# Optimization experiments

Hardware: AMD Instinct MI355X
Metric: run time of the kernel (lower is better)

## Reference

```python
import jax, jax.numpy as jnp
import numpy as np


def _layernorm(x, g, b, eps=1e-5):
    mu = x.mean(-1, keepdims=True)
    var = ((x - mu) ** 2).mean(-1, keepdims=True)
    return (x - mu) / jnp.sqrt(var + eps) * g + b


def _bilinear_sample(feat, coords):
    # feat: (B,C,H,W,D); coords: (B,C,N,2) normalized to [-1,1]
    # torch.grid_sample(mode='bilinear', padding_mode='zeros', align_corners=True)
    B, C, H, W, D = feat.shape
    x = (coords[..., 0] + 1.0) * 0.5 * (W - 1)  # grid x -> width axis
    y = (coords[..., 1] + 1.0) * 0.5 * (H - 1)  # grid y -> height axis
    x0 = jnp.floor(x)
    y0 = jnp.floor(y)
    wx1 = x - x0
    wy1 = y - y0
    bi = jnp.arange(B)[:, None, None]
    ci = jnp.arange(C)[None, :, None]

    def corner(yi, xi, w):
        inb = (xi >= 0) & (xi < W) & (yi >= 0) & (yi < H)
        xc = jnp.clip(xi, 0, W - 1).astype(jnp.int32)
        yc = jnp.clip(yi, 0, H - 1).astype(jnp.int32)
        v = feat[bi, ci, yc, xc]  # (B,C,N,D) gather
        return v * (w * inb)[..., None]

    return (corner(y0, x0, (1 - wy1) * (1 - wx1))
            + corner(y0, x0 + 1, (1 - wy1) * wx1)
            + corner(y0 + 1, x0, wy1 * (1 - wx1))
            + corner(y0 + 1, x0 + 1, wy1 * wx1))


def setup_inputs() -> dict:
    key = jax.random.key(0)
    ks = jax.random.split(key, 12)
    B, C, N, D, H, W = 2, 8, 16384, 256, 64, 64
    s = 1.0 / np.sqrt(D).astype(np.float32)
    return {
        "queries": jax.random.normal(ks[0], (B, N, D), jnp.float32),
        "image_features": jax.random.normal(ks[1], (B, C, H, W, D), jnp.float32),
        "pixel_coords": jax.random.uniform(ks[2], (B, C, N, 2), jnp.float32) * 2.0 - 1.0,
        "valid_mask": jax.random.randint(ks[3], (B, C, N), 0, 2).astype(jnp.int32),
        "Wq": jax.random.normal(ks[4], (D, D), jnp.float32) * s,
        "bq": jnp.zeros((D,), jnp.float32),
        "Wkv": jax.random.normal(ks[5], (D, 2 * D), jnp.float32) * s,
        "bkv": jnp.zeros((2 * D,), jnp.float32),
        "Wo": jax.random.normal(ks[6], (D, D), jnp.float32) * s,
        "bo": jnp.zeros((D,), jnp.float32),
        "gamma": jnp.ones((D,), jnp.float32),
        "beta": jnp.zeros((D,), jnp.float32),
    }


def reference(queries, image_features, pixel_coords, valid_mask,
              Wq, bq, Wkv, bkv, Wo, bo, gamma, beta):
    B, N, D = queries.shape
    residual = queries
    qn = _layernorm(queries, gamma, beta)
    sampled = _bilinear_sample(image_features, pixel_coords)      # (B,C,N,D)
    sampled = jnp.transpose(sampled, (0, 2, 1, 3))                 # (B,N,C,D)
    q = qn @ Wq + bq                                               # (B,N,D)
    kv = sampled @ Wkv + bkv                                       # (B,N,C,2D)
    k, v = kv[..., :D], kv[..., D:]
    scores = jnp.einsum('bnd,bncd->bnc', q, k) / jnp.sqrt(jnp.float32(D))
    valid = jnp.transpose(valid_mask, (0, 2, 1)) != 0              # (B,N,C)
    scores = jnp.where(valid, scores, -jnp.inf)
    attn = jax.nn.softmax(scores, axis=-1)
    attn = jnp.where(jnp.isnan(attn), 0.0, attn)                   # all-invalid -> 0
    out = jnp.einsum('bnc,bncd->bnd', attn, v)
    return residual + out @ Wo + bo
```

## Files before the change

### kernel.cpp

```cpp
#include <hip/hip_runtime.h>
#include <math.h>

#define NROWS 32768

typedef __attribute__((ext_vector_type(8))) short short8;
typedef __attribute__((ext_vector_type(4))) float f32x4;

#define WS_ABF    0
#define WS_WVOBF  32768
#define WS_PB     65536
#define WS_BVO    65792
#define WS_FEATBF 8487424

__device__ __forceinline__ unsigned short f2bf(float f) {
    unsigned u = __builtin_bit_cast(unsigned, f);
    u += 0x7FFFu + ((u >> 16) & 1u);
    return (unsigned short)(u >> 16);
}
__device__ __forceinline__ float bf_lo(unsigned u) {
    return __builtin_bit_cast(float, u << 16);
}
__device__ __forceinline__ float bf_hi(unsigned u) {
    return __builtin_bit_cast(float, u & 0xFFFF0000u);
}

__global__ __launch_bounds__(256)
void precompute_kernel(const float* __restrict__ Wq, const float* __restrict__ bq,
                       const float* __restrict__ Wkv, const float* __restrict__ bkv,
                       const float* __restrict__ Wo, const float* __restrict__ feat,
                       float* __restrict__ ws) {
    int t = threadIdx.x;
    int blk = blockIdx.x;
    if (blk >= 514) {
        long i = (long)(blk - 514) * 4096 + t * 16;
        const float4* src = (const float4*)(feat + i);
        unsigned short* dst = (unsigned short*)(ws + WS_FEATBF) + i;
        #pragma unroll
        for (int h = 0; h < 2; ++h) {
            float4 a = src[2 * h], b = src[2 * h + 1];
            uint4 o;
            o.x = (unsigned)f2bf(a.x) | ((unsigned)f2bf(a.y) << 16);
            o.y = (unsigned)f2bf(a.z) | ((unsigned)f2bf(a.w) << 16);
            o.z = (unsigned)f2bf(b.x) | ((unsigned)f2bf(b.y) << 16);
            o.w = (unsigned)f2bf(b.z) | ((unsigned)f2bf(b.w) << 16);
            *(uint4*)(dst + 8 * h) = o;
        }
        return;
    }
    if (blk < 256) {
        int f = blk;
        const float4* wq4 = (const float4*)(Wq + f * 256);
        const float4* wk4 = (const float4*)(Wkv + (long)t * 512);
        float acc = 0.f;
        #pragma unroll 8
        for (int d4 = 0; d4 < 64; ++d4) {
            float4 a = wq4[d4], b = wk4[d4];
            acc += a.x * b.x + a.y * b.y + a.z * b.z + a.w * b.w;
        }
        ((unsigned short*)(ws + WS_ABF))[t * 256 + f] = f2bf(acc);
    } else if (blk < 512) {
        int e = blk - 256;
        float acc = 0.f;
        #pragma unroll 8
        for (int g = 0; g < 256; ++g)
            acc = fmaf(Wkv[(long)e * 512 + 256 + g], Wo[g * 256 + t], acc);
        ((unsigned short*)(ws + WS_WVOBF))[t * 256 + e] = f2bf(acc);
    } else if (blk == 512) {
        float acc = 0.f;
        #pragma unroll 8
        for (int d = 0; d < 256; ++d)
            acc = fmaf(bq[d], Wkv[(long)t * 512 + d], acc);
        ws[WS_PB + t] = acc;
    } else {
        float acc = 0.f;
        #pragma unroll 8
        for (int g = 0; g < 256; ++g)
            acc = fmaf(bkv[256 + g], Wo[g * 256 + t], acc);
        ws[WS_BVO + t] = acc;
    }
}

#define RPB  32
#define SLOT 260

__global__ __launch_bounds__(512, 8)
void fused_rowpipe(const float* __restrict__ queries, const float* __restrict__ gamma,
                   const float* __restrict__ beta, const float* __restrict__ coords,
                   const int* __restrict__ vmask, const float* __restrict__ bo,
                   const float* __restrict__ ws, float* __restrict__ out) {
    __shared__ float buf[RPB * SLOT + RPB];
    float* ssu = buf + RPB * SLOT;

    const unsigned short* Abf    = (const unsigned short*)(ws + WS_ABF);
    const unsigned short* Wvobf  = (const unsigned short*)(ws + WS_WVOBF);
    const float*          pb     = ws + WS_PB;
    const float*          bvo    = ws + WS_BVO;
    const unsigned short* featbf = (const unsigned short*)(ws + WS_FEATBF);

    int tid = threadIdx.x, wave = tid >> 6, lane = tid & 63;
    long row0 = (long)blockIdx.x * RPB;

    float4 qstash[4];

    {
        float4 g4 = *(const float4*)(gamma + 4 * lane);
        float4 b4 = *(const float4*)(beta + 4 * lane);
        #pragma unroll
        for (int rr = 0; rr < 4; ++rr) {
            int r = wave * 4 + rr;
            float4 v = *(const float4*)(queries + (row0 + r) * 256 + 4 * lane);
            qstash[rr] = v;
            float s = v.x + v.y + v.z + v.w;
            s += __shfl_xor(s, 32); s += __shfl_xor(s, 16); s += __shfl_xor(s, 8);
            s += __shfl_xor(s, 4);  s += __shfl_xor(s, 2);  s += __shfl_xor(s, 1);
            float mu = s * 0.00390625f;
            float dx = v.x - mu, dy = v.y - mu, dz = v.z - mu, dw = v.w - mu;
            float vv = dx * dx + dy * dy + dz * dz + dw * dw;
            vv += __shfl_xor(vv, 32); vv += __shfl_xor(vv, 16); vv += __shfl_xor(vv, 8);
            vv += __shfl_xor(vv, 4);  vv += __shfl_xor(vv, 2);  vv += __shfl_xor(vv, 1);
            float rstd = rsqrtf(vv * 0.00390625f + 1e-5f);
            float qx = dx * rstd * g4.x + b4.x;
            float qy = dy * rstd * g4.y + b4.y;
            float qz = dz * rstd * g4.z + b4.z;
            float qw = dw * rstd * g4.w + b4.w;
            unsigned lo = (unsigned)f2bf(qx) | ((unsigned)f2bf(qy) << 16);
            unsigned hi = (unsigned)f2bf(qz) | ((unsigned)f2bf(qw) << 16);
            *(uint2*)((unsigned short*)&buf[r * SLOT] + 4 * lane) = make_uint2(lo, hi);
        }
    }
    __syncthreads();

    int r16 = lane & 15, g = lane >> 4;
    f32x4 zero = {0.f, 0.f, 0.f, 0.f};

    {
        f32x4 acc[2][2];
        #pragma unroll
        for (int mt = 0; mt < 2; ++mt)
            #pragma unroll
            for (int nt = 0; nt < 2; ++nt) acc[mt][nt] = zero;

        #pragma unroll
        for (int ks = 0; ks < 8; ++ks) {
            short8 bfr[2], afr[2];
            #pragma unroll
            for (int nt = 0; nt < 2; ++nt)
                bfr[nt] = *(const short8*)(Abf + ((wave * 32 + nt * 16 + r16) << 8) + ks * 32 + g * 8);
            #pragma unroll
            for (int mt = 0; mt < 2; ++mt)
                afr[mt] = *(const short8*)((const unsigned short*)buf + (mt * 16 + r16) * (SLOT * 2) + ks * 32 + g * 8);
            #pragma unroll
            for (int mt = 0; mt < 2; ++mt)
                #pragma unroll
                for (int nt = 0; nt < 2; ++nt)
                    acc[mt][nt] = __builtin_amdgcn_mfma_f32_16x16x32_bf16(afr[mt], bfr[nt], acc[mt][nt], 0, 0, 0);
        }
        __syncthreads();

        float pbv[2];
        #pragma unroll
        for (int nt = 0; nt < 2; ++nt) pbv[nt] = pb[wave * 32 + nt * 16 + r16];
        #pragma unroll
        for (int mt = 0; mt < 2; ++mt)
            #pragma unroll
            for (int nt = 0; nt < 2; ++nt)
                #pragma unroll
                for (int rg = 0; rg < 4; ++rg)
                    buf[(mt * 16 + g * 4 + rg) * SLOT + wave * 32 + nt * 16 + r16] =
                        acc[mt][nt][rg] + pbv[nt];
    }
    __syncthreads();

    for (int rr = 0; rr < 4; ++rr) {
        int r = wave * 4 + rr;
        int rowu = __builtin_amdgcn_readfirstlane((int)(row0 + r));
        int b = rowu >> 14;
        int n = rowu & 16383;

        float4 p4 = *(const float4*)(&buf[r * SLOT + 4 * lane]);

        float m = -INFINITY, ssum = 0.f;
        float4 sbacc = {0.f, 0.f, 0.f, 0.f};

        #pragma unroll
        for (int c = 0; c < 8; ++c) {
            long cb = (long)(b * 8 + c) * 16384 + n;
            float cx = coords[2 * cb];
            float cy = coords[2 * cb + 1];
            bool vld = (vmask[cb] != 0);
            float x = (cx + 1.f) * 31.5f;
            float y = (cy + 1.f) * 31.5f;
            float x0f = floorf(x), y0f = floorf(y);
            float wx = x - x0f, wy = y - y0f;
            int ix0 = (int)x0f, iy0 = (int)y0f;
            int ix1 = ix0 + 1, iy1 = iy0 + 1;
            float bx0 = (ix0 >= 0 && ix0 < 64) ? 1.f : 0.f;
            float bx1 = (ix1 >= 0 && ix1 < 64) ? 1.f : 0.f;
            float by0 = (iy0 >= 0 && iy0 < 64) ? 1.f : 0.f;
            float by1 = (iy1 >= 0 && iy1 < 64) ? 1.f : 0.f;
            int cx0 = min(max(ix0, 0), 63), cx1 = min(max(ix1, 0), 63);
            int cy0 = min(max(iy0, 0), 63), cy1 = min(max(iy1, 0), 63);
            const unsigned short* fb = featbf + ((long)(b * 8 + c) << 20);
            const uint2* r00 = (const uint2*)(fb + ((cy0 * 64 + cx0) << 8)) + lane;
            const uint2* r01 = (const uint2*)(fb + ((cy0 * 64 + cx1) << 8)) + lane;
            const uint2* r10 = (const uint2*)(fb + ((cy1 * 64 + cx0) << 8)) + lane;
            const uint2* r11 = (const uint2*)(fb + ((cy1 * 64 + cx1) << 8)) + lane;
            float w00 = (1.f - wy) * (1.f - wx) * by0 * bx0;
            float w01 = (1.f - wy) * wx * by0 * bx1;
            float w10 = wy * (1.f - wx) * by1 * bx0;
            float w11 = wy * wx * by1 * bx1;
            uint2 v00 = *r00, v01 = *r01, v10 = *r10, v11 = *r11;
            float4 s;
            s.x = w00 * bf_lo(v00.x) + w01 * bf_lo(v01.x) + w10 * bf_lo(v10.x) + w11 * bf_lo(v11.x);
            s.y = w00 * bf_hi(v00.x) + w01 * bf_hi(v01.x) + w10 * bf_hi(v10.x) + w11 * bf_hi(v11.x);
            s.z = w00 * bf_lo(v00.y) + w01 * bf_lo(v01.y) + w10 * bf_lo(v10.y) + w11 * bf_lo(v11.y);
            s.w = w00 * bf_hi(v00.y) + w01 * bf_hi(v01.y) + w10 * bf_hi(v10.y) + w11 * bf_hi(v11.y);
            float t = s.x * p4.x + s.y * p4.y + s.z * p4.z + s.w * p4.w;
            t += __shfl_xor(t, 32); t += __shfl_xor(t, 16); t += __shfl_xor(t, 8);
            t += __shfl_xor(t, 4);  t += __shfl_xor(t, 2);  t += __shfl_xor(t, 1);
            t *= 0.0625f;
            if (vld) {
                float nm = fmaxf(m, t);
                float scale = __expf(m - nm);
                float w = __expf(t - nm);
                ssum = ssum * scale + w;
                sbacc.x = fmaf(w, s.x, sbacc.x * scale);
                sbacc.y = fmaf(w, s.y, sbacc.y * scale);
                sbacc.z = fmaf(w, s.z, sbacc.z * scale);
                sbacc.w = fmaf(w, s.w, sbacc.w * scale);
                m = nm;
            }
        }

        float4 sb = {0.f, 0.f, 0.f, 0.f};
        float sa = 0.f;
        if (m > -INFINITY) {
            float inv = 1.f / ssum;
            sb.x = sbacc.x * inv;
            sb.y = sbacc.y * inv;
            sb.z = sbacc.z * inv;
            sb.w = sbacc.w * inv;
            sa = 1.f;
        }
        unsigned lo = (unsigned)f2bf(sb.x) | ((unsigned)f2bf(sb.y) << 16);
        unsigned hi = (unsigned)f2bf(sb.z) | ((unsigned)f2bf(sb.w) << 16);
        *(uint2*)((unsigned short*)&buf[r * SLOT] + 4 * lane) = make_uint2(lo, hi);
        if (lane == 0) ssu[r] = sa;
    }
    __syncthreads();

    {
        f32x4 acc2[2][2];
        #pragma unroll
        for (int mt = 0; mt < 2; ++mt)
            #pragma unroll
            for (int nt = 0; nt < 2; ++nt) acc2[mt][nt] = zero;

        #pragma unroll
        for (int ks = 0; ks < 8; ++ks) {
            short8 bfr[2], afr[2];
            #pragma unroll
            for (int nt = 0; nt < 2; ++nt)
                bfr[nt] = *(const short8*)(Wvobf + ((wave * 32 + nt * 16 + r16) << 8) + ks * 32 + g * 8);
            #pragma unroll
            for (int mt = 0; mt < 2; ++mt)
                afr[mt] = *(const short8*)((const unsigned short*)buf + (mt * 16 + r16) * (SLOT * 2) + ks * 32 + g * 8);
            #pragma unroll
            for (int mt = 0; mt < 2; ++mt)
                #pragma unroll
                for (int nt = 0; nt < 2; ++nt)
                    acc2[mt][nt] = __builtin_amdgcn_mfma_f32_16x16x32_bf16(afr[mt], bfr[nt], acc2[mt][nt], 0, 0, 0);
        }
        __syncthreads();

        #pragma unroll
        for (int mt = 0; mt < 2; ++mt)
            #pragma unroll
            for (int nt = 0; nt < 2; ++nt)
                #pragma unroll
                for (int rg = 0; rg < 4; ++rg)
                    buf[(mt * 16 + g * 4 + rg) * SLOT + wave * 32 + nt * 16 + r16] = acc2[mt][nt][rg];
    }
    __syncthreads();

    {
        float4 bvo4 = *(const float4*)(bvo + 4 * lane);
        float4 bo4  = *(const float4*)(bo + 4 * lane);
        #pragma unroll
        for (int rr = 0; rr < 4; ++rr) {
            int r = wave * 4 + rr;
            float4 q4 = qstash[rr];
            float4 a4 = *(const float4*)(&buf[r * SLOT + 4 * lane]);
            float su = ssu[r];
            float4 o;
            o.x = q4.x + a4.x + su * bvo4.x + bo4.x;
            o.y = q4.y + a4.y + su * bvo4.y + bo4.y;
            o.z = q4.z + a4.z + su * bvo4.z + bo4.z;
            o.w = q4.w + a4.w + su * bvo4.w + bo4.w;
            *(float4*)(out + (row0 + r) * 256 + 4 * lane) = o;
        }
    }
}

extern "C" void kernel_launch(void* const* d_in, const int* in_sizes, int n_in,
                              void* d_out, int out_size, void* d_ws, size_t ws_size,
                              hipStream_t stream) {
    const float* queries = (const float*)d_in[0];
    const float* feat    = (const float*)d_in[1];
    const float* coords  = (const float*)d_in[2];
    const int*   vmask   = (const int*)  d_in[3];
    const float* Wq      = (const float*)d_in[4];
    const float* bq      = (const float*)d_in[5];
    const float* Wkv     = (const float*)d_in[6];
    const float* bkv     = (const float*)d_in[7];
    const float* Wo      = (const float*)d_in[8];
    const float* bo      = (const float*)d_in[9];
    const float* gamma   = (const float*)d_in[10];
    const float* beta    = (const float*)d_in[11];
    float* out = (float*)d_out;
    float* ws  = (float*)d_ws;

    precompute_kernel<<<514 + 4096, 256, 0, stream>>>(Wq, bq, Wkv, bkv, Wo, feat, ws);
    fused_rowpipe<<<NROWS / RPB, 512, 0, stream>>>(queries, gamma, beta, coords, vmask, bo, ws, out);
}
```

Baseline: 267.5 us.

## Process two rows per wave with 16-byte gathers and branchless online softmax

The sampling/softmax stage now splits each wavefront into two 32-lane halves. Each half handles its own row and gathers 8 bf16 values per lane with 16-byte loads instead of 4 with 8-byte loads. This halves the loop iterations per wave, cuts the shuffle reduction by one step, and replaces the divergent valid-branch with predicated selects. The 1/sqrt(D) scale is folded into the projected query and bias, and the bf16 feature buffer offset in the workspace is moved to sit right after the small tensors. Register pressure rises from the wider per-lane accumulators.

```diff
diff --git a/kernel.cpp b/kernel.cpp
--- a/kernel.cpp
+++ b/kernel.cpp
@@ -10,7 +10,7 @@
 #define WS_WVOBF  32768
 #define WS_PB     65536
 #define WS_BVO    65792
-#define WS_FEATBF 8487424
+#define WS_FEATBF 66048
 
 __device__ __forceinline__ unsigned short f2bf(float f) {
     unsigned u = __builtin_bit_cast(unsigned, f);
@@ -70,7 +70,7 @@
         #pragma unroll 8
         for (int d = 0; d < 256; ++d)
             acc = fmaf(bq[d], Wkv[(long)t * 512 + d], acc);
-        ws[WS_PB + t] = acc;
+        ws[WS_PB + t] = acc * 0.0625f;
     } else {
         float acc = 0.f;
         #pragma unroll 8
@@ -167,85 +167,90 @@
                 #pragma unroll
                 for (int rg = 0; rg < 4; ++rg)
                     buf[(mt * 16 + g * 4 + rg) * SLOT + wave * 32 + nt * 16 + r16] =
-                        acc[mt][nt][rg] + pbv[nt];
+                        acc[mt][nt][rg] * 0.0625f + pbv[nt];
     }
     __syncthreads();
 
-    for (int rr = 0; rr < 4; ++rr) {
-        int r = wave * 4 + rr;
-        int rowu = __builtin_amdgcn_readfirstlane((int)(row0 + r));
-        int b = rowu >> 14;
-        int n = rowu & 16383;
-
-        float4 p4 = *(const float4*)(&buf[r * SLOT + 4 * lane]);
-
-        float m = -INFINITY, ssum = 0.f;
-        float4 sbacc = {0.f, 0.f, 0.f, 0.f};
-
-        #pragma unroll
-        for (int c = 0; c < 8; ++c) {
-            long cb = (long)(b * 8 + c) * 16384 + n;
-            float cx = coords[2 * cb];
-            float cy = coords[2 * cb + 1];
-            bool vld = (vmask[cb] != 0);
-            float x = (cx + 1.f) * 31.5f;
-            float y = (cy + 1.f) * 31.5f;
-            float x0f = floorf(x), y0f = floorf(y);
-            float wx = x - x0f, wy = y - y0f;
-            int ix0 = (int)x0f, iy0 = (int)y0f;
-            int ix1 = ix0 + 1, iy1 = iy0 + 1;
-            float bx0 = (ix0 >= 0 && ix0 < 64) ? 1.f : 0.f;
-            float bx1 = (ix1 >= 0 && ix1 < 64) ? 1.f : 0.f;
-            float by0 = (iy0 >= 0 && iy0 < 64) ? 1.f : 0.f;
-            float by1 = (iy1 >= 0 && iy1 < 64) ? 1.f : 0.f;
-            int cx0 = min(max(ix0, 0), 63), cx1 = min(max(ix1, 0), 63);
-            int cy0 = min(max(iy0, 0), 63), cy1 = min(max(iy1, 0), 63);
-            const unsigned short* fb = featbf + ((long)(b * 8 + c) << 20);
-            const uint2* r00 = (const uint2*)(fb + ((cy0 * 64 + cx0) << 8)) + lane;
-            const uint2* r01 = (const uint2*)(fb + ((cy0 * 64 + cx1) << 8)) + lane;
-            const uint2* r10 = (const uint2*)(fb + ((cy1 * 64 + cx0) << 8)) + lane;
-            const uint2* r11 = (const uint2*)(fb + ((cy1 * 64 + cx1) << 8)) + lane;
-            float w00 = (1.f - wy) * (1.f - wx) * by0 * bx0;
-            float w01 = (1.f - wy) * wx * by0 * bx1;
-            float w10 = wy * (1.f - wx) * by1 * bx0;
-            float w11 = wy * wx * by1 * bx1;
-            uint2 v00 = *r00, v01 = *r01, v10 = *r10, v11 = *r11;
-            float4 s;
-            s.x = w00 * bf_lo(v00.x) + w01 * bf_lo(v01.x) + w10 * bf_lo(v10.x) + w11 * bf_lo(v11.x);
-            s.y = w00 * bf_hi(v00.x) + w01 * bf_hi(v01.x) + w10 * bf_hi(v10.x) + w11 * bf_hi(v11.x);
-            s.z = w00 * bf_lo(v00.y) + w01 * bf_lo(v01.y) + w10 * bf_lo(v10.y) + w11 * bf_lo(v11.y);
-            s.w = w00 * bf_hi(v00.y) + w01 * bf_hi(v01.y) + w10 * bf_hi(v10.y) + w11 * bf_hi(v11.y);
-            float t = s.x * p4.x + s.y * p4.y + s.z * p4.z + s.w * p4.w;
-            t += __shfl_xor(t, 32); t += __shfl_xor(t, 16); t += __shfl_xor(t, 8);
-            t += __shfl_xor(t, 4);  t += __shfl_xor(t, 2);  t += __shfl_xor(t, 1);
-            t *= 0.0625f;
-            if (vld) {
-                float nm = fmaxf(m, t);
-                float scale = __expf(m - nm);
-                float w = __expf(t - nm);
+    {
+        int half = lane >> 5, l5 = lane & 31;
+        #pragma unroll
+        for (int it = 0; it < 2; ++it) {
+            int r = wave * 4 + it * 2 + half;
+            long rowl = row0 + r;
+            int b = (int)(rowl >> 14);
+            int n = (int)(rowl & 16383);
+
+            float4 pA = *(const float4*)(&buf[r * SLOT + 8 * l5]);
+            float4 pB = *(const float4*)(&buf[r * SLOT + 8 * l5 + 4]);
+
+            float m = -INFINITY, ssum = 0.f;
+            float4 sA = {0.f, 0.f, 0.f, 0.f}, sB = {0.f, 0.f, 0.f, 0.f};
+
+            #pragma unroll
+            for (int c = 0; c < 8; ++c) {
+                long cb = (long)(b * 8 + c) * 16384 + n;
+                float cx = coords[2 * cb];
+                float cy = coords[2 * cb + 1];
+                bool vld = (vmask[cb] != 0);
+                float x = (cx + 1.f) * 31.5f;
+                float y = (cy + 1.f) * 31.5f;
+                float x0f = floorf(x), y0f = floorf(y);
+                float wx = x - x0f, wy = y - y0f;
+                int ix0 = (int)x0f, iy0 = (int)y0f;
+                int ix1 = ix0 + 1, iy1 = iy0 + 1;
+                float bx0 = (ix0 >= 0 && ix0 < 64) ? 1.f : 0.f;
+                float bx1 = (ix1 >= 0 && ix1 < 64) ? 1.f : 0.f;
+                float by0 = (iy0 >= 0 && iy0 < 64) ? 1.f : 0.f;
+                float by1 = (iy1 >= 0 && iy1 < 64) ? 1.f : 0.f;
+                int cx0 = min(max(ix0, 0), 63), cx1 = min(max(ix1, 0), 63);
+                int cy0 = min(max(iy0, 0), 63), cy1 = min(max(iy1, 0), 63);
+                const unsigned short* fb = featbf + ((long)(b * 8 + c) << 20);
+                uint4 v00 = *((const uint4*)(fb + ((cy0 * 64 + cx0) << 8)) + l5);
+                uint4 v01 = *((const uint4*)(fb + ((cy0 * 64 + cx1) << 8)) + l5);
+                uint4 v10 = *((const uint4*)(fb + ((cy1 * 64 + cx0) << 8)) + l5);
+                uint4 v11 = *((const uint4*)(fb + ((cy1 * 64 + cx1) << 8)) + l5);
+                float w00 = (1.f - wy) * (1.f - wx) * by0 * bx0;
+                float w01 = (1.f - wy) * wx * by0 * bx1;
+                float w10 = wy * (1.f - wx) * by1 * bx0;
+                float w11 = wy * wx * by1 * bx1;
+                float s0 = w00*bf_lo(v00.x) + w01*bf_lo(v01.x) + w10*bf_lo(v10.x) + w11*bf_lo(v11.x);
+                float s1 = w00*bf_hi(v00.x) + w01*bf_hi(v01.x) + w10*bf_hi(v10.x) + w11*bf_hi(v11.x);
+                float s2 = w00*bf_lo(v00.y) + w01*bf_lo(v01.y) + w10*bf_lo(v10.y) + w11*bf_lo(v11.y);
+                float s3 = w00*bf_hi(v00.y) + w01*bf_hi(v01.y) + w10*bf_hi(v10.y) + w11*bf_hi(v11.y);
+                float s4 = w00*bf_lo(v00.z) + w01*bf_lo(v01.z) + w10*bf_lo(v10.z) + w11*bf_lo(v11.z);
+                float s5 = w00*bf_hi(v00.z) + w01*bf_hi(v01.z) + w10*bf_hi(v10.z) + w11*bf_hi(v11.z);
+                float s6 = w00*bf_lo(v00.w) + w01*bf_lo(v01.w) + w10*bf_lo(v10.w) + w11*bf_lo(v11.w);
+                float s7 = w00*bf_hi(v00.w) + w01*bf_hi(v01.w) + w10*bf_hi(v10.w) + w11*bf_hi(v11.w);
+                float t = s0 * pA.x + s1 * pA.y + s2 * pA.z + s3 * pA.w
+                        + s4 * pB.x + s5 * pB.y + s6 * pB.z + s7 * pB.w;
+                t += __shfl_xor(t, 16); t += __shfl_xor(t, 8); t += __shfl_xor(t, 4);
+                t += __shfl_xor(t, 2);  t += __shfl_xor(t, 1);
+                float nm = vld ? fmaxf(m, t) : m;
+                float d  = (m > -INFINITY) ? (m - nm) : 0.f;
+                float scale = __expf(d);
+                float w = vld ? __expf(t - nm) : 0.f;
                 ssum = ssum * scale + w;
-                sbacc.x = fmaf(w, s.x, sbacc.x * scale);
-                sbacc.y = fmaf(w, s.y, sbacc.y * scale);
-                sbacc.z = fmaf(w, s.z, sbacc.z * scale);
-                sbacc.w = fmaf(w, s.w, sbacc.w * scale);
+                sA.x = fmaf(w, s0, sA.x * scale);
+                sA.y = fmaf(w, s1, sA.y * scale);
+                sA.z = fmaf(w, s2, sA.z * scale);
+                sA.w = fmaf(w, s3, sA.w * scale);
+                sB.x = fmaf(w, s4, sB.x * scale);
+                sB.y = fmaf(w, s5, sB.y * scale);
+                sB.z = fmaf(w, s6, sB.z * scale);
+                sB.w = fmaf(w, s7, sB.w * scale);
                 m = nm;
             }
-        }
-
-        float4 sb = {0.f, 0.f, 0.f, 0.f};
-        float sa = 0.f;
-        if (m > -INFINITY) {
-            float inv = 1.f / ssum;
-            sb.x = sbacc.x * inv;
-            sb.y = sbacc.y * inv;
-            sb.z = sbacc.z * inv;
-            sb.w = sbacc.w * inv;
-            sa = 1.f;
-        }
-        unsigned lo = (unsigned)f2bf(sb.x) | ((unsigned)f2bf(sb.y) << 16);
-        unsigned hi = (unsigned)f2bf(sb.z) | ((unsigned)f2bf(sb.w) << 16);
-        *(uint2*)((unsigned short*)&buf[r * SLOT] + 4 * lane) = make_uint2(lo, hi);
-        if (lane == 0) ssu[r] = sa;
+
+            float inv = (m > -INFINITY) ? (1.f / ssum) : 0.f;
+            float sa  = (m > -INFINITY) ? 1.f : 0.f;
+            uint4 o;
+            o.x = (unsigned)f2bf(sA.x * inv) | ((unsigned)f2bf(sA.y * inv) << 16);
+            o.y = (unsigned)f2bf(sA.z * inv) | ((unsigned)f2bf(sA.w * inv) << 16);
+            o.z = (unsigned)f2bf(sB.x * inv) | ((unsigned)f2bf(sB.y * inv) << 16);
+            o.w = (unsigned)f2bf(sB.z * inv) | ((unsigned)f2bf(sB.w * inv) << 16);
+            *(uint4*)((unsigned short*)&buf[r * SLOT] + 8 * l5) = o;
+            if (l5 == 0) ssu[r] = sa;
+        }
     }
     __syncthreads();
 
```

Result: slower. 673.8 us (+151.9%).
